# Optimization experiments

Measured on AMD Instinct MI355X. Metric: run time of the kernel, lower is better.

## Reference

```python
import jax, jax.numpy as jnp
import numpy as np

P = 64
K = 64
D = 2048
KERNEL_MUL = 2.0
KERNEL_NUM = 5


def setup_inputs() -> dict:
    key = jax.random.key(0)
    k1, k2 = jax.random.split(key)
    source = jax.random.normal(k1, (P * K, D), dtype=jnp.float32)
    target = jax.random.normal(k2, (P * K, D), dtype=jnp.float32)
    return {"source": source, "target": target}


def _mmd_terms(source, target):
    # split into P groups of K rows each, process all splits at once
    src = source.reshape(P, K, D)
    tgt = target.reshape(P, K, D)
    total = jnp.concatenate([src, tgt], axis=1)          # [P, 2K, D]
    n = 2 * K
    # pairwise squared L2 distances per split: [P, 2K, 2K]
    sq = jnp.sum(total * total, axis=-1)                  # [P, 2K]
    gram = jnp.einsum('pid,pjd->pij', total, total)       # [P, 2K, 2K]
    l2 = sq[:, :, None] + sq[:, None, :] - 2.0 * gram
    # bandwidth from detached distances (torch uses L2_distance.data)
    bw = jax.lax.stop_gradient(jnp.sum(l2, axis=(1, 2))) / (n * n - n)  # [P]
    bw = bw / (KERNEL_MUL ** (KERNEL_NUM // 2))
    mults = KERNEL_MUL ** jnp.arange(KERNEL_NUM, dtype=jnp.float32)     # [kn]
    bws = bw[:, None] * mults[None, :] + 1e-9                           # [P, kn]
    # multi-bandwidth Gaussian kernel sum: [P, 2K, 2K]
    kern = jnp.sum(jnp.exp(-l2[:, None, :, :] / bws[:, :, None, None]), axis=1)
    XX = kern[:, :K, :K]
    YY = kern[:, K:, K:]
    XY = kern[:, :K, K:]
    YX = kern[:, K:, :K]
    xx = jnp.mean(XX, axis=(1, 2))
    yy = jnp.mean(YY, axis=(1, 2))
    xy = jnp.mean(XY, axis=(1, 2))
    yx = jnp.mean(YX, axis=(1, 2))
    per_split_loss = xx + yy - xy - yx                    # [P]
    total_loss = jnp.sum(per_split_loss) / P
    return total_loss, l2, xx, yy, xy, yx


def reference(source, target):
    total_loss, l2, xx, yy, xy, yx = _mmd_terms(source, target)
    # original returns max of l2dist from the LAST split only
    max_l2_last = jnp.max(l2[-1])
    return (total_loss.reshape(1), max_l2_last,
            jnp.sum(xx) / P, jnp.sum(yy) / P, jnp.sum(xy) / P, jnp.sum(yx) / P)
```

## Files before the change

### kernel.cpp

```cpp
#include <hip/hip_runtime.h>

typedef _Float16 half8 __attribute__((ext_vector_type(8)));
typedef float floatx4 __attribute__((ext_vector_type(4)));
typedef unsigned int uint2v __attribute__((ext_vector_type(2)));

#define NSPLIT 64
#define KS 64
#define DIM 2048
#define NROW 128
#define BK 128
#define NKC (DIM / BK)
#define SST 152
#define GST 129

__device__ __forceinline__ unsigned int pk16(float a, float b) {
  return __builtin_bit_cast(unsigned int, __builtin_amdgcn_cvt_pkrtz(a, b));
}

__global__ void init_out_kernel(float* out) {
  if (threadIdx.x < 6) out[threadIdx.x] = 0.0f;
}

__global__ __launch_bounds__(1024) void mmd_kernel(const float* __restrict__ src,
                                                   const float* __restrict__ tgt,
                                                   float* __restrict__ out) {
  __shared__ __align__(16) _Float16 stage[NROW * SST];
  __shared__ __align__(16) float gram[NROW * GST];
  __shared__ float sqv[NROW];
  __shared__ float reds[16];
  __shared__ float redm[16];
  __shared__ float quad[4];
  __shared__ float bcast[8];

  const int p = blockIdx.x;
  const int tid = threadIdx.x;
  const int lane = tid & 63;
  const int wave = tid >> 6;

  const int srow = tid >> 3;
  const int c4 = (tid & 7) * 4;
  const float* rowp = (srow < KS) ? (src + (size_t)(p * KS + srow) * DIM)
                                  : (tgt + (size_t)(p * KS + (srow - KS)) * DIM);

  const int wr = (wave >> 2) * 32;
  const int wc = (wave & 3) * 32;
  const int fr = lane & 15;
  const int fk = (lane >> 4) * 8;

  floatx4 acc00 = {0.f, 0.f, 0.f, 0.f};
  floatx4 acc01 = {0.f, 0.f, 0.f, 0.f};
  floatx4 acc10 = {0.f, 0.f, 0.f, 0.f};
  floatx4 acc11 = {0.f, 0.f, 0.f, 0.f};

  float4 f0, f1, f2, f3;
#define LOADK(kc)                                      \
  do {                                                 \
    const float* gp_ = rowp + (kc) * BK + c4;          \
    f0 = *(const float4*)(gp_);                        \
    f1 = *(const float4*)(gp_ + 32);                   \
    f2 = *(const float4*)(gp_ + 64);                   \
    f3 = *(const float4*)(gp_ + 96);                   \
  } while (0)

  LOADK(0);
  for (int kc = 0; kc < NKC; ++kc) {
    __syncthreads();
    {
      _Float16* sp = &stage[srow * SST + c4];
      *(uint2v*)(sp)      = (uint2v){pk16(f0.x, f0.y), pk16(f0.z, f0.w)};
      *(uint2v*)(sp + 32) = (uint2v){pk16(f1.x, f1.y), pk16(f1.z, f1.w)};
      *(uint2v*)(sp + 64) = (uint2v){pk16(f2.x, f2.y), pk16(f2.z, f2.w)};
      *(uint2v*)(sp + 96) = (uint2v){pk16(f3.x, f3.y), pk16(f3.z, f3.w)};
    }
    __syncthreads();
    if (kc + 1 < NKC) LOADK(kc + 1);
#pragma unroll
    for (int ks = 0; ks < 4; ++ks) {
      const int ko = ks * 32 + fk;
      half8 a0 = *(const half8*)&stage[(wr + fr) * SST + ko];
      half8 a1 = *(const half8*)&stage[(wr + 16 + fr) * SST + ko];
      half8 b0 = *(const half8*)&stage[(wc + fr) * SST + ko];
      half8 b1 = *(const half8*)&stage[(wc + 16 + fr) * SST + ko];
      acc00 = __builtin_amdgcn_mfma_f32_16x16x32_f16(a0, b0, acc00, 0, 0, 0);
      acc01 = __builtin_amdgcn_mfma_f32_16x16x32_f16(a0, b1, acc01, 0, 0, 0);
      acc10 = __builtin_amdgcn_mfma_f32_16x16x32_f16(a1, b0, acc10, 0, 0, 0);
      acc11 = __builtin_amdgcn_mfma_f32_16x16x32_f16(a1, b1, acc11, 0, 0, 0);
    }
  }
#undef LOADK

  {
    const int ccol = lane & 15;
    const int crow = (lane >> 4) * 4;
#pragma unroll
    for (int r = 0; r < 4; ++r) {
      gram[(wr + crow + r) * GST + (wc + ccol)] = acc00[r];
      gram[(wr + crow + r) * GST + (wc + 16 + ccol)] = acc01[r];
      gram[(wr + 16 + crow + r) * GST + (wc + ccol)] = acc10[r];
      gram[(wr + 16 + crow + r) * GST + (wc + 16 + ccol)] = acc11[r];
    }
  }
  if (tid < 4) quad[tid] = 0.0f;
  __syncthreads();

  if (tid < NROW) sqv[tid] = gram[tid * GST + tid];
  __syncthreads();

  const int row = tid >> 3;
  const int c0 = (tid & 7) * 16;
  float l2r[16];
  float lsum = 0.0f;
  float lmax = -1e30f;
  const float sqi = sqv[row];
#pragma unroll
  for (int m = 0; m < 16; ++m) {
    float g = gram[row * GST + c0 + m];
    float v = sqi + sqv[c0 + m] - 2.0f * g;
    l2r[m] = v;
    lsum += v;
    lmax = fmaxf(lmax, v);
  }
#pragma unroll
  for (int m = 1; m <= 32; m <<= 1) {
    lsum += __shfl_xor(lsum, m, 64);
    lmax = fmaxf(lmax, __shfl_xor(lmax, m, 64));
  }
  if (lane == 0) {
    reds[wave] = lsum;
    redm[wave] = lmax;
  }
  __syncthreads();
  if (tid == 0) {
    float tot = 0.0f, mx = -1e30f;
    for (int w = 0; w < 16; ++w) {
      tot += reds[w];
      mx = fmaxf(mx, redm[w]);
    }
    float bw = tot / (float)(NROW * NROW - NROW) * 0.25f;
    float mult = 1.0f;
    for (int k = 0; k < 5; ++k) {
      bcast[k] = 1.0f / (bw * mult + 1e-9f);
      mult *= 2.0f;
    }
    if (p == NSPLIT - 1) out[1] = mx;
  }
  __syncthreads();

  const float ib0 = bcast[0], ib1 = bcast[1], ib2 = bcast[2], ib3 = bcast[3], ib4 = bcast[4];
  float qsum = 0.0f;
#pragma unroll
  for (int m = 0; m < 16; ++m) {
    float v = l2r[m];
    qsum += __expf(-v * ib0) + __expf(-v * ib1) + __expf(-v * ib2) +
            __expf(-v * ib3) + __expf(-v * ib4);
  }
  qsum += __shfl_xor(qsum, 1, 64);
  qsum += __shfl_xor(qsum, 2, 64);
  qsum += __shfl_xor(qsum, 8, 64);
  qsum += __shfl_xor(qsum, 16, 64);
  qsum += __shfl_xor(qsum, 32, 64);
  if (lane == 0 || lane == 4) {
    int q = (wave >= 8 ? 2 : 0) + ((lane >> 2) & 1);
    atomicAdd(&quad[q], qsum);
  }
  __syncthreads();

  if (tid == 0) {
    const float inv = 1.0f / (4096.0f * 64.0f);
    float xx = quad[0], xy = quad[1], yx = quad[2], yy = quad[3];
    atomicAdd(&out[0], (xx + yy - xy - yx) * inv);
    atomicAdd(&out[2], xx * inv);
    atomicAdd(&out[3], yy * inv);
    atomicAdd(&out[4], xy * inv);
    atomicAdd(&out[5], yx * inv);
  }
}

extern "C" void kernel_launch(void* const* d_in, const int* in_sizes, int n_in,
                              void* d_out, int out_size, void* d_ws, size_t ws_size,
                              hipStream_t stream) {
  const float* src = (const float*)d_in[0];
  const float* tgt = (const float*)d_in[1];
  float* out = (float*)d_out;
  init_out_kernel<<<1, 64, 0, stream>>>(out);
  mmd_kernel<<<NSPLIT, 1024, 0, stream>>>(src, tgt, out);
}
```

Before: 120.6 us.

## Split Gram computation along feature dim across four blocks, reduce in second kernel

Splits the per-group Gram matrix computation into four K-chunks, each handled by a separate block, which raises the grid from 64 to 256 blocks on a GPU with many more CUs. Partial Gram matrices are written to workspace and summed by a new reduce kernel that then runs the distance, bandwidth and exponential-kernel reductions. This adds a kernel launch and about 16 MB of workspace traffic.

Measured after the change: 112.8 us. 6.5% less time.

```diff
diff --git a/kernel.cpp b/kernel.cpp
--- a/kernel.cpp
+++ b/kernel.cpp
@@ -9,9 +9,11 @@
 #define DIM 2048
 #define NROW 128
 #define BK 128
-#define NKC (DIM / BK)
+#define KSPL 4
+#define KCH (DIM / KSPL)
+#define NKC_A (KCH / BK)
 #define SST 152
-#define GST 129
+#define GSZ (NROW * NROW)
 
 __device__ __forceinline__ unsigned int pk16(float a, float b) {
   return __builtin_bit_cast(unsigned int, __builtin_amdgcn_cvt_pkrtz(a, b));
@@ -21,26 +23,22 @@
   if (threadIdx.x < 6) out[threadIdx.x] = 0.0f;
 }
 
-__global__ __launch_bounds__(1024) void mmd_kernel(const float* __restrict__ src,
-                                                   const float* __restrict__ tgt,
-                                                   float* __restrict__ out) {
+__global__ __launch_bounds__(1024) void gram_kernel(const float* __restrict__ src,
+                                                    const float* __restrict__ tgt,
+                                                    float* __restrict__ ws) {
   __shared__ __align__(16) _Float16 stage[NROW * SST];
-  __shared__ __align__(16) float gram[NROW * GST];
-  __shared__ float sqv[NROW];
-  __shared__ float reds[16];
-  __shared__ float redm[16];
-  __shared__ float quad[4];
-  __shared__ float bcast[8];
-
-  const int p = blockIdx.x;
+
+  const int p = blockIdx.x >> 2;
+  const int c = blockIdx.x & (KSPL - 1);
   const int tid = threadIdx.x;
   const int lane = tid & 63;
   const int wave = tid >> 6;
 
   const int srow = tid >> 3;
   const int c4 = (tid & 7) * 4;
-  const float* rowp = (srow < KS) ? (src + (size_t)(p * KS + srow) * DIM)
-                                  : (tgt + (size_t)(p * KS + (srow - KS)) * DIM);
+  const float* rowp = ((srow < KS) ? (src + (size_t)(p * KS + srow) * DIM)
+                                   : (tgt + (size_t)(p * KS + (srow - KS)) * DIM)) +
+                      c * KCH;
 
   const int wr = (wave >> 2) * 32;
   const int wc = (wave & 3) * 32;
@@ -63,7 +61,7 @@
   } while (0)
 
   LOADK(0);
-  for (int kc = 0; kc < NKC; ++kc) {
+  for (int kc = 0; kc < NKC_A; ++kc) {
     __syncthreads();
     {
       _Float16* sp = &stage[srow * SST + c4];
@@ -73,7 +71,7 @@
       *(uint2v*)(sp + 96) = (uint2v){pk16(f3.x, f3.y), pk16(f3.z, f3.w)};
     }
     __syncthreads();
-    if (kc + 1 < NKC) LOADK(kc + 1);
+    if (kc + 1 < NKC_A) LOADK(kc + 1);
 #pragma unroll
     for (int ks = 0; ks < 4; ++ks) {
       const int ko = ks * 32 + fk;
@@ -89,33 +87,62 @@
   }
 #undef LOADK
 
-  {
-    const int ccol = lane & 15;
-    const int crow = (lane >> 4) * 4;
-#pragma unroll
-    for (int r = 0; r < 4; ++r) {
-      gram[(wr + crow + r) * GST + (wc + ccol)] = acc00[r];
-      gram[(wr + crow + r) * GST + (wc + 16 + ccol)] = acc01[r];
-      gram[(wr + 16 + crow + r) * GST + (wc + ccol)] = acc10[r];
-      gram[(wr + 16 + crow + r) * GST + (wc + 16 + ccol)] = acc11[r];
-    }
-  }
-  if (tid < 4) quad[tid] = 0.0f;
-  __syncthreads();
-
-  if (tid < NROW) sqv[tid] = gram[tid * GST + tid];
-  __syncthreads();
+  float* wsp = ws + (size_t)blockIdx.x * GSZ;
+  const int ccol = lane & 15;
+  const int crow = (lane >> 4) * 4;
+#pragma unroll
+  for (int r = 0; r < 4; ++r) {
+    wsp[(wr + crow + r) * NROW + (wc + ccol)] = acc00[r];
+    wsp[(wr + crow + r) * NROW + (wc + 16 + ccol)] = acc01[r];
+    wsp[(wr + 16 + crow + r) * NROW + (wc + ccol)] = acc10[r];
+    wsp[(wr + 16 + crow + r) * NROW + (wc + 16 + ccol)] = acc11[r];
+  }
+}
+
+__global__ __launch_bounds__(1024) void reduce_kernel(const float* __restrict__ ws,
+                                                      float* __restrict__ out) {
+  __shared__ float sqv[NROW];
+  __shared__ float reds[16];
+  __shared__ float redm[16];
+  __shared__ float quad[4];
+  __shared__ float bcast[8];
+
+  const int p = blockIdx.x;
+  const int tid = threadIdx.x;
+  const int lane = tid & 63;
+  const int wave = tid >> 6;
 
   const int row = tid >> 3;
   const int c0 = (tid & 7) * 16;
+
+  const float* base = ws + (size_t)p * KSPL * GSZ + row * NROW + c0;
+  float4 g0 = {0.f, 0.f, 0.f, 0.f}, g1 = g0, g2 = g0, g3 = g0;
+#pragma unroll
+  for (int c = 0; c < KSPL; ++c) {
+    const float* bp = base + (size_t)c * GSZ;
+    float4 t0 = *(const float4*)(bp);
+    float4 t1 = *(const float4*)(bp + 4);
+    float4 t2 = *(const float4*)(bp + 8);
+    float4 t3 = *(const float4*)(bp + 12);
+    g0.x += t0.x; g0.y += t0.y; g0.z += t0.z; g0.w += t0.w;
+    g1.x += t1.x; g1.y += t1.y; g1.z += t1.z; g1.w += t1.w;
+    g2.x += t2.x; g2.y += t2.y; g2.z += t2.z; g2.w += t2.w;
+    g3.x += t3.x; g3.y += t3.y; g3.z += t3.z; g3.w += t3.w;
+  }
+  float gs[16] = {g0.x, g0.y, g0.z, g0.w, g1.x, g1.y, g1.z, g1.w,
+                  g2.x, g2.y, g2.z, g2.w, g3.x, g3.y, g3.z, g3.w};
+
+  if ((tid & 7) == (row >> 4)) sqv[row] = gs[row & 15];
+  if (tid < 4) quad[tid] = 0.0f;
+  __syncthreads();
+
   float l2r[16];
   float lsum = 0.0f;
   float lmax = -1e30f;
   const float sqi = sqv[row];
 #pragma unroll
   for (int m = 0; m < 16; ++m) {
-    float g = gram[row * GST + c0 + m];
-    float v = sqi + sqv[c0 + m] - 2.0f * g;
+    float v = sqi + sqv[c0 + m] - 2.0f * gs[m];
     l2r[m] = v;
     lsum += v;
     lmax = fmaxf(lmax, v);
@@ -182,6 +209,8 @@
   const float* src = (const float*)d_in[0];
   const float* tgt = (const float*)d_in[1];
   float* out = (float*)d_out;
+  float* ws = (float*)d_ws;
   init_out_kernel<<<1, 64, 0, stream>>>(out);
-  mmd_kernel<<<NSPLIT, 1024, 0, stream>>>(src, tgt, out);
-}
+  gram_kernel<<<NSPLIT * KSPL, 1024, 0, stream>>>(src, tgt, ws);
+  reduce_kernel<<<NSPLIT, 1024, 0, stream>>>(ws, out);
+}
```
